# Optimization experiments

Hardware: AMD Instinct MI355X
Metric: run time of the kernel (lower is better)

## Reference

```python
import jax, jax.numpy as jnp
import numpy as np


def setup_inputs() -> dict:
    key = jax.random.key(0)
    k1, k2 = jax.random.split(key)
    x = jax.random.normal(k1, (131072, 256), dtype=jnp.float32)
    centroids = jax.random.normal(k2, (2048, 256), dtype=jnp.float32)
    return {"x": x, "centroids": centroids}


def reference(x, centroids):
    """One k-means step: L2 nearest-centroid assignment + scatter-mean update.

    x:         (n, d) sample vectors
    centroids: (K, d) current centroids
    returns:   (K, d) new centroids
    """
    K = centroids.shape[0]
    # Squared L2 distance argmin; ||x||^2 term is constant per row, drop it.
    # scores[n, K] = ||c_k||^2 - 2 * x_n . c_k
    c_sq = jnp.sum(centroids * centroids, axis=-1)          # (K,)
    scores = c_sq[None, :] - 2.0 * jnp.einsum("nd,kd->nk", x, centroids)
    assigns = jnp.argmin(scores, axis=-1)                    # (n,) int
    # Segment mean update; keep old centroid for empty clusters.
    sums = jax.ops.segment_sum(x, assigns, num_segments=K)   # (K, d)
    counts = jax.ops.segment_sum(jnp.ones((x.shape[0],), x.dtype), assigns,
                                 num_segments=K)             # (K,)
    nonempty = counts > 0
    means = sums / jnp.maximum(counts, 1.0)[:, None]
    new_centroids = jnp.where(nonempty[:, None], means, centroids)
    return new_centroids
```

## Files before the change

### kernel.cpp

```cpp
#include <hip/hip_runtime.h>

typedef unsigned short u16;
typedef unsigned int u32;
typedef __attribute__((ext_vector_type(4)))  int  i32x4;
typedef __attribute__((ext_vector_type(16))) int  i32x16;
typedef __attribute__((ext_vector_type(16))) char i8x16;

#define NPTS 131072
#define DIM  256
#define KC   2048

constexpr float S1  = 0.0625f;
constexpr float S2  = S1 / 254.0f;
constexpr float S3  = S2 * S2 / S1;
constexpr float IS1 = 16.0f;
constexpr float IS2 = 4064.0f;
constexpr float IS3 = 1.0f / S3;
constexpr float W_A = S1 * S1;
constexpr float R2  = 1.0f / 254.0f;
constexpr float R3  = 1.0f / 64516.0f;

__device__ inline void quant3(float v, char& q1, char& q2, char& q3) {
    float a = fminf(fmaxf(rintf(v * IS1), -127.f), 127.f);
    float r1 = fmaf(-a, S1, v);
    float b = fminf(fmaxf(rintf(r1 * IS2), -127.f), 127.f);
    float r2 = fmaf(-b, S2, r1);
    float c = fminf(fmaxf(rintf(r2 * IS3), -127.f), 127.f);
    q1 = (char)a; q2 = (char)b; q3 = (char)c;
}

#define GLD16(gsrc, ldst) \
    __builtin_amdgcn_global_load_lds( \
        (const __attribute__((address_space(1))) void*)(gsrc), \
        (__attribute__((address_space(3))) void*)(ldst), 16, 0, 0)

__global__ void cprep_kernel(const float* __restrict__ cen,
                             char* __restrict__ c_q,
                             float* __restrict__ c_sq,
                             int* __restrict__ hist) {
    if (blockIdx.x < 8) hist[blockIdx.x * 256 + threadIdx.x] = 0;
    const int lane = threadIdx.x & 63;
    const int wv   = threadIdx.x >> 6;
    const int n    = blockIdx.x * 4 + wv;
    float4 v = ((const float4*)(cen + (size_t)n * DIM))[lane];
    float ss = v.x * v.x + v.y * v.y + v.z * v.z + v.w * v.w;
    float fv[4] = {v.x, v.y, v.z, v.w};
    char q1[4], q2[4], q3[4];
#pragma unroll
    for (int j = 0; j < 4; ++j) quant3(fv[j], q1[j], q2[j], q3[j]);
    const int g = n >> 5, r32 = n & 31;
    const int s = lane >> 2;
    const size_t base = ((size_t)((g * 16 + s) * 32 + r32)) * 16 + (lane & 3) * 4;
    u32 p1 = (u32)(unsigned char)q1[0] | ((u32)(unsigned char)q1[1] << 8) |
             ((u32)(unsigned char)q1[2] << 16) | ((u32)(unsigned char)q1[3] << 24);
    u32 p2 = (u32)(unsigned char)q2[0] | ((u32)(unsigned char)q2[1] << 8) |
             ((u32)(unsigned char)q2[2] << 16) | ((u32)(unsigned char)q2[3] << 24);
    u32 p3 = (u32)(unsigned char)q3[0] | ((u32)(unsigned char)q3[1] << 8) |
             ((u32)(unsigned char)q3[2] << 16) | ((u32)(unsigned char)q3[3] << 24);
    *(u32*)(c_q + base) = p1;
    *(u32*)(c_q + (size_t)KC * DIM + base) = p2;
    *(u32*)(c_q + (size_t)2 * KC * DIM + base) = p3;
#pragma unroll
    for (int off = 32; off > 0; off >>= 1) ss += __shfl_xor(ss, off);
    if (lane == 0) c_sq[n] = 0.5f * ss / W_A;
}

__global__ __launch_bounds__(256, 3) void assign_kernel(
    const float* __restrict__ x, const char* __restrict__ c_q,
    const float* __restrict__ c_sq, int* __restrict__ assigns,
    int* __restrict__ hist) {
    __shared__ char lds_c[2 * 24576];

    const int tid  = threadIdx.x;
    const int lane = tid & 63;
    const int wv   = tid >> 6;
    const int l31  = lane & 31;
    const int kh   = lane >> 5;

    const int m = blockIdx.x * 128 + wv * 32 + l31;
    const float4* xr = (const float4*)(x + (size_t)m * DIM);
    i8x16 xq1[8], xq2[8], xq3[8];
#pragma unroll
    for (int kt = 0; kt < 8; ++kt) {
        float tmp[16];
#pragma unroll
        for (int j = 0; j < 4; ++j) {
            float4 f = xr[kt * 8 + kh * 4 + j];
            tmp[j * 4 + 0] = f.x; tmp[j * 4 + 1] = f.y;
            tmp[j * 4 + 2] = f.z; tmp[j * 4 + 3] = f.w;
        }
        i8x16 v1, v2, v3;
#pragma unroll
        for (int j = 0; j < 16; ++j) {
            char a, b, c;
            quant3(tmp[j], a, b, c);
            v1[j] = a; v2[j] = b; v3[j] = c;
        }
        xq1[kt] = v1; xq2[kt] = v2; xq3[kt] = v3;
    }

    const float4* csq4 = (const float4*)c_sq;
    float best = 3.4e38f;
    int bidx = 0;

    const char* cl2 = c_q + (size_t)KC * DIM;
    const char* cl3 = c_q + (size_t)2 * KC * DIM;
    {
        GLD16(c_q + tid * 16,         lds_c + tid * 16);
        GLD16(c_q + (tid + 256) * 16, lds_c + (tid + 256) * 16);
        GLD16(cl2 + tid * 16,         lds_c + 8192 + tid * 16);
        GLD16(cl2 + (tid + 256) * 16, lds_c + 8192 + (tid + 256) * 16);
        GLD16(cl3 + tid * 16,         lds_c + 16384 + tid * 16);
        GLD16(cl3 + (tid + 256) * 16, lds_c + 16384 + (tid + 256) * 16);
    }

    for (int nt = 0; nt < 64; ++nt) {
        const int b = nt & 1;
        __syncthreads();
        if (nt < 63) {
            const size_t so = (size_t)(nt + 1) * 8192;
            char* d = lds_c + (b ^ 1) * 24576;
            GLD16(c_q + so + tid * 16,         d + tid * 16);
            GLD16(c_q + so + (tid + 256) * 16, d + (tid + 256) * 16);
            GLD16(cl2 + so + tid * 16,         d + 8192 + tid * 16);
            GLD16(cl2 + so + (tid + 256) * 16, d + 8192 + (tid + 256) * 16);
            GLD16(cl3 + so + tid * 16,         d + 16384 + tid * 16);
            GLD16(cl3 + so + (tid + 256) * 16, d + 16384 + (tid + 256) * 16);
        }

        i32x16 accA = {}, accB = {}, accC = {};
        const char* cb = lds_c + b * 24576;
#pragma unroll
        for (int kt = 0; kt < 8; ++kt) {
            const int off = ((kt * 2 + kh) * 32 + l31) * 16;
            i32x4 c1 = __builtin_bit_cast(i32x4, *(const i8x16*)(cb + off));
            i32x4 c2 = __builtin_bit_cast(i32x4, *(const i8x16*)(cb + 8192 + off));
            i32x4 c3 = __builtin_bit_cast(i32x4, *(const i8x16*)(cb + 16384 + off));
            i32x4 x1 = __builtin_bit_cast(i32x4, xq1[kt]);
            i32x4 x2 = __builtin_bit_cast(i32x4, xq2[kt]);
            i32x4 x3 = __builtin_bit_cast(i32x4, xq3[kt]);
            accA = __builtin_amdgcn_mfma_i32_32x32x32_i8(c1, x1, accA, 0, 0, 0);
            accB = __builtin_amdgcn_mfma_i32_32x32x32_i8(c1, x2, accB, 0, 0, 0);
            accC = __builtin_amdgcn_mfma_i32_32x32x32_i8(c2, x2, accC, 0, 0, 0);
            accB = __builtin_amdgcn_mfma_i32_32x32x32_i8(c2, x1, accB, 0, 0, 0);
            accC = __builtin_amdgcn_mfma_i32_32x32x32_i8(c1, x3, accC, 0, 0, 0);
            accC = __builtin_amdgcn_mfma_i32_32x32x32_i8(c3, x1, accC, 0, 0, 0);
        }

#pragma unroll
        for (int bq = 0; bq < 4; ++bq) {
            float4 cs = csq4[nt * 8 + 2 * bq + kh];
            const int n0 = nt * 32 + 8 * bq + 4 * kh;
            float csa[4] = {cs.x, cs.y, cs.z, cs.w};
#pragma unroll
            for (int r = 0; r < 4; ++r) {
                const int idx = bq * 4 + r;
                float dot = fmaf((float)accB[idx], R2,
                            fmaf((float)accC[idx], R3, (float)accA[idx]));
                float v = csa[r] - dot;
                if (v < best) { best = v; bidx = n0 + r; }
            }
        }
    }

    float oval = __shfl_xor(best, 32);
    int   oidx = __shfl_xor(bidx, 32);
    if (oval < best || (oval == best && oidx < bidx)) { best = oval; bidx = oidx; }
    if (lane < 32) {
        assigns[m] = bidx;
        atomicAdd(&hist[bidx], 1);
    }
}

__global__ void scan_kernel(const int* __restrict__ hist,
                            int* __restrict__ base_,
                            int* __restrict__ cursor) {
    __shared__ int tmp[256];
    const int tid = threadIdx.x;
    int v[8], s = 0;
#pragma unroll
    for (int j = 0; j < 8; ++j) { v[j] = hist[tid * 8 + j]; s += v[j]; }
    tmp[tid] = s;
    __syncthreads();
    for (int off = 1; off < 256; off <<= 1) {
        int t = (tid >= off) ? tmp[tid - off] : 0;
        __syncthreads();
        tmp[tid] += t;
        __syncthreads();
    }
    int ex = tmp[tid] - s;
#pragma unroll
    for (int j = 0; j < 8; ++j) {
        base_[tid * 8 + j] = ex;
        cursor[tid * 8 + j] = ex;
        ex += v[j];
    }
}

__global__ void reorder_kernel(const int* __restrict__ assigns,
                               int* __restrict__ cursor,
                               int* __restrict__ order) {
    const int p = blockIdx.x * 256 + threadIdx.x;
    const int a = assigns[p];
    int pos = atomicAdd(&cursor[a], 1);
    order[pos] = p;
}

__global__ void reduce_kernel(const float* __restrict__ x,
                              const int* __restrict__ order,
                              const int* __restrict__ assigns,
                              float* __restrict__ sums) {
    const int tid = threadIdx.x;
    const int r0 = blockIdx.x * 256;
    float acc = 0.f;
    int cur = assigns[order[r0]];
    for (int r = 0; r < 256; r += 4) {
        int p0 = order[r0 + r + 0], p1 = order[r0 + r + 1];
        int p2 = order[r0 + r + 2], p3 = order[r0 + r + 3];
        float v0 = x[(size_t)p0 * DIM + tid];
        float v1 = x[(size_t)p1 * DIM + tid];
        float v2 = x[(size_t)p2 * DIM + tid];
        float v3 = x[(size_t)p3 * DIM + tid];
        int a0 = assigns[p0], a1 = assigns[p1], a2 = assigns[p2], a3 = assigns[p3];
        if (a0 != cur) { unsafeAtomicAdd(&sums[(size_t)cur * DIM + tid], acc); acc = 0.f; cur = a0; }
        acc += v0;
        if (a1 != cur) { unsafeAtomicAdd(&sums[(size_t)cur * DIM + tid], acc); acc = 0.f; cur = a1; }
        acc += v1;
        if (a2 != cur) { unsafeAtomicAdd(&sums[(size_t)cur * DIM + tid], acc); acc = 0.f; cur = a2; }
        acc += v2;
        if (a3 != cur) { unsafeAtomicAdd(&sums[(size_t)cur * DIM + tid], acc); acc = 0.f; cur = a3; }
        acc += v3;
    }
    unsafeAtomicAdd(&sums[(size_t)cur * DIM + tid], acc);
}

__global__ void finalize_kernel(const float* __restrict__ sums,
                                const int* __restrict__ hist,
                                const float* __restrict__ cen,
                                float* __restrict__ out) {
    const int id = blockIdx.x * 256 + threadIdx.x;
    const int k = id >> 6;
    const int cnt = hist[k];
    float4 s = ((const float4*)sums)[id];
    float4 c = ((const float4*)cen)[id];
    float4 o;
    if (cnt > 0) {
        float r = 1.0f / (float)cnt;
        o.x = s.x * r; o.y = s.y * r; o.z = s.z * r; o.w = s.w * r;
    } else {
        o = c;
    }
    ((float4*)out)[id] = o;
}

extern "C" void kernel_launch(void* const* d_in, const int* in_sizes, int n_in,
                              void* d_out, int out_size, void* d_ws, size_t ws_size,
                              hipStream_t stream) {
    (void)in_sizes; (void)n_in; (void)out_size; (void)ws_size;
    const float* x   = (const float*)d_in[0];
    const float* cen = (const float*)d_in[1];
    float* out = (float*)d_out;

    char* ws = (char*)d_ws;
    size_t off = 0;
    char* c_q = (char*)(ws + off);           off += (size_t)3 * KC * DIM;
    float* c_sq = (float*)(ws + off);        off += (size_t)KC * 4;
    int* assigns = (int*)(ws + off);         off += (size_t)NPTS * 4;
    int* hist = (int*)(ws + off);            off += (size_t)KC * 4;
    int* base_ = (int*)(ws + off);           off += (size_t)KC * 4;
    int* cursor = (int*)(ws + off);          off += (size_t)KC * 4;
    int* order = (int*)(ws + off);           off += (size_t)NPTS * 4;
    float* sums = (float*)(ws + off);        off += (size_t)KC * DIM * 4;

    hipMemsetAsync(sums, 0, (size_t)KC * DIM * sizeof(float), stream);
    cprep_kernel<<<KC / 4, 256, 0, stream>>>(cen, c_q, c_sq, hist);
    assign_kernel<<<NPTS / 128, 256, 0, stream>>>(x, c_q, c_sq, assigns, hist);
    scan_kernel<<<1, 256, 0, stream>>>(hist, base_, cursor);
    reorder_kernel<<<NPTS / 256, 256, 0, stream>>>(assigns, cursor, order);
    reduce_kernel<<<NPTS / 256, 256, 0, stream>>>(x, order, assigns, sums);
    finalize_kernel<<<KC * 64 / 256, 256, 0, stream>>>(sums, hist, cen, out);
}
```

Before: 610.5 us.

## Halve LDS staging with half-tile double buffering, fuse sums memset into cprep

```diff
diff --git a/kernel.cpp b/kernel.cpp
--- a/kernel.cpp
+++ b/kernel.cpp
@@ -17,15 +17,14 @@
 constexpr float IS2 = 4064.0f;
 constexpr float IS3 = 1.0f / S3;
 constexpr float W_A = S1 * S1;
-constexpr float R2  = 1.0f / 254.0f;
 constexpr float R3  = 1.0f / 64516.0f;
 
 __device__ inline void quant3(float v, char& q1, char& q2, char& q3) {
     float a = fminf(fmaxf(rintf(v * IS1), -127.f), 127.f);
     float r1 = fmaf(-a, S1, v);
-    float b = fminf(fmaxf(rintf(r1 * IS2), -127.f), 127.f);
+    float b = rintf(r1 * IS2);
     float r2 = fmaf(-b, S2, r1);
-    float c = fminf(fmaxf(rintf(r2 * IS3), -127.f), 127.f);
+    float c = rintf(r2 * IS3);
     q1 = (char)a; q2 = (char)b; q3 = (char)c;
 }
 
@@ -37,8 +36,11 @@
 __global__ void cprep_kernel(const float* __restrict__ cen,
                              char* __restrict__ c_q,
                              float* __restrict__ c_sq,
-                             int* __restrict__ hist) {
+                             int* __restrict__ hist,
+                             float* __restrict__ sums) {
     if (blockIdx.x < 8) hist[blockIdx.x * 256 + threadIdx.x] = 0;
+    float4 z = {0.f, 0.f, 0.f, 0.f};
+    ((float4*)sums)[blockIdx.x * 256 + threadIdx.x] = z;
     const int lane = threadIdx.x & 63;
     const int wv   = threadIdx.x >> 6;
     const int n    = blockIdx.x * 4 + wv;
@@ -65,11 +67,11 @@
     if (lane == 0) c_sq[n] = 0.5f * ss / W_A;
 }
 
-__global__ __launch_bounds__(256, 3) void assign_kernel(
+__global__ __launch_bounds__(256, 4) void assign_kernel(
     const float* __restrict__ x, const char* __restrict__ c_q,
     const float* __restrict__ c_sq, int* __restrict__ assigns,
     int* __restrict__ hist) {
-    __shared__ char lds_c[2 * 24576];
+    __shared__ char lds_c[2 * 12288];
 
     const int tid  = threadIdx.x;
     const int lane = tid & 63;
@@ -105,58 +107,56 @@
 
     const char* cl2 = c_q + (size_t)KC * DIM;
     const char* cl3 = c_q + (size_t)2 * KC * DIM;
-    {
-        GLD16(c_q + tid * 16,         lds_c + tid * 16);
-        GLD16(c_q + (tid + 256) * 16, lds_c + (tid + 256) * 16);
-        GLD16(cl2 + tid * 16,         lds_c + 8192 + tid * 16);
-        GLD16(cl2 + (tid + 256) * 16, lds_c + 8192 + (tid + 256) * 16);
-        GLD16(cl3 + tid * 16,         lds_c + 16384 + tid * 16);
-        GLD16(cl3 + (tid + 256) * 16, lds_c + 16384 + (tid + 256) * 16);
-    }
-
-    for (int nt = 0; nt < 64; ++nt) {
-        const int b = nt & 1;
-        __syncthreads();
-        if (nt < 63) {
-            const size_t so = (size_t)(nt + 1) * 8192;
-            char* d = lds_c + (b ^ 1) * 24576;
-            GLD16(c_q + so + tid * 16,         d + tid * 16);
-            GLD16(c_q + so + (tid + 256) * 16, d + (tid + 256) * 16);
-            GLD16(cl2 + so + tid * 16,         d + 8192 + tid * 16);
-            GLD16(cl2 + so + (tid + 256) * 16, d + 8192 + (tid + 256) * 16);
-            GLD16(cl3 + so + tid * 16,         d + 16384 + tid * 16);
-            GLD16(cl3 + so + (tid + 256) * 16, d + 16384 + (tid + 256) * 16);
-        }
-
+
+#define DMA_SUB(dstbuf, srcoff) do { \
+        char* _d = lds_c + (dstbuf) * 12288; \
+        const size_t _o = (srcoff); \
+        GLD16(c_q + _o + tid * 16, _d + tid * 16); \
+        GLD16(cl2 + _o + tid * 16, _d + 4096 + tid * 16); \
+        GLD16(cl3 + _o + tid * 16, _d + 8192 + tid * 16); \
+    } while (0)
+
+#define KSTEP(b, ktl, xi) do { \
+        const char* _cb = lds_c + (b) * 12288; \
+        const int _off = (((ktl) * 2 + kh) * 32 + l31) * 16; \
+        i32x4 c1 = __builtin_bit_cast(i32x4, *(const i8x16*)(_cb + _off)); \
+        i32x4 c2 = __builtin_bit_cast(i32x4, *(const i8x16*)(_cb + 4096 + _off)); \
+        i32x4 c3 = __builtin_bit_cast(i32x4, *(const i8x16*)(_cb + 8192 + _off)); \
+        i32x4 x1 = __builtin_bit_cast(i32x4, xq1[xi]); \
+        i32x4 x2 = __builtin_bit_cast(i32x4, xq2[xi]); \
+        i32x4 x3 = __builtin_bit_cast(i32x4, xq3[xi]); \
+        accA = __builtin_amdgcn_mfma_i32_32x32x32_i8(c1, x1, accA, 0, 0, 0); \
+        accB = __builtin_amdgcn_mfma_i32_32x32x32_i8(c1, x2, accB, 0, 0, 0); \
+        accC = __builtin_amdgcn_mfma_i32_32x32x32_i8(c2, x2, accC, 0, 0, 0); \
+        accB = __builtin_amdgcn_mfma_i32_32x32x32_i8(c2, x1, accB, 0, 0, 0); \
+        accC = __builtin_amdgcn_mfma_i32_32x32x32_i8(c1, x3, accC, 0, 0, 0); \
+        accC = __builtin_amdgcn_mfma_i32_32x32x32_i8(c3, x1, accC, 0, 0, 0); \
+    } while (0)
+
+    DMA_SUB(0, 0);
+
+    int buf = 0;
+    for (int g = 0; g < 64; ++g) {
+        __syncthreads();
+        DMA_SUB(buf ^ 1, (size_t)g * 8192 + 4096);
         i32x16 accA = {}, accB = {}, accC = {};
-        const char* cb = lds_c + b * 24576;
-#pragma unroll
-        for (int kt = 0; kt < 8; ++kt) {
-            const int off = ((kt * 2 + kh) * 32 + l31) * 16;
-            i32x4 c1 = __builtin_bit_cast(i32x4, *(const i8x16*)(cb + off));
-            i32x4 c2 = __builtin_bit_cast(i32x4, *(const i8x16*)(cb + 8192 + off));
-            i32x4 c3 = __builtin_bit_cast(i32x4, *(const i8x16*)(cb + 16384 + off));
-            i32x4 x1 = __builtin_bit_cast(i32x4, xq1[kt]);
-            i32x4 x2 = __builtin_bit_cast(i32x4, xq2[kt]);
-            i32x4 x3 = __builtin_bit_cast(i32x4, xq3[kt]);
-            accA = __builtin_amdgcn_mfma_i32_32x32x32_i8(c1, x1, accA, 0, 0, 0);
-            accB = __builtin_amdgcn_mfma_i32_32x32x32_i8(c1, x2, accB, 0, 0, 0);
-            accC = __builtin_amdgcn_mfma_i32_32x32x32_i8(c2, x2, accC, 0, 0, 0);
-            accB = __builtin_amdgcn_mfma_i32_32x32x32_i8(c2, x1, accB, 0, 0, 0);
-            accC = __builtin_amdgcn_mfma_i32_32x32x32_i8(c1, x3, accC, 0, 0, 0);
-            accC = __builtin_amdgcn_mfma_i32_32x32x32_i8(c3, x1, accC, 0, 0, 0);
-        }
+        KSTEP(buf, 0, 0); KSTEP(buf, 1, 1); KSTEP(buf, 2, 2); KSTEP(buf, 3, 3);
+        buf ^= 1;
+        __syncthreads();
+        if (g < 63) DMA_SUB(buf ^ 1, (size_t)(g + 1) * 8192);
+        KSTEP(buf, 0, 4); KSTEP(buf, 1, 5); KSTEP(buf, 2, 6); KSTEP(buf, 3, 7);
+        buf ^= 1;
 
 #pragma unroll
         for (int bq = 0; bq < 4; ++bq) {
-            float4 cs = csq4[nt * 8 + 2 * bq + kh];
-            const int n0 = nt * 32 + 8 * bq + 4 * kh;
+            float4 cs = csq4[g * 8 + 2 * bq + kh];
+            const int n0 = g * 32 + 8 * bq + 4 * kh;
             float csa[4] = {cs.x, cs.y, cs.z, cs.w};
 #pragma unroll
             for (int r = 0; r < 4; ++r) {
                 const int idx = bq * 4 + r;
-                float dot = fmaf((float)accB[idx], R2,
-                            fmaf((float)accC[idx], R3, (float)accA[idx]));
+                int bc = __mul24(accB[idx], 254) + accC[idx];
+                float dot = fmaf((float)bc, R3, (float)accA[idx]);
                 float v = csa[r] - dot;
                 if (v < best) { best = v; bidx = n0 + r; }
             }
@@ -170,6 +170,8 @@
         assigns[m] = bidx;
         atomicAdd(&hist[bidx], 1);
     }
+#undef DMA_SUB
+#undef KSTEP
 }
 
 __global__ void scan_kernel(const int* __restrict__ hist,
@@ -272,8 +274,7 @@
     int* order = (int*)(ws + off);           off += (size_t)NPTS * 4;
     float* sums = (float*)(ws + off);        off += (size_t)KC * DIM * 4;
 
-    hipMemsetAsync(sums, 0, (size_t)KC * DIM * sizeof(float), stream);
-    cprep_kernel<<<KC / 4, 256, 0, stream>>>(cen, c_q, c_sq, hist);
+    cprep_kernel<<<KC / 4, 256, 0, stream>>>(cen, c_q, c_sq, hist, sums);
     assign_kernel<<<NPTS / 128, 256, 0, stream>>>(x, c_q, c_sq, assigns, hist);
     scan_kernel<<<1, 256, 0, stream>>>(hist, base_, cursor);
     reorder_kernel<<<NPTS / 256, 256, 0, stream>>>(assigns, cursor, order);
```

Result: slower. 787.4 us (+29.0%).
